# Optimization experiments

Hardware: AMD Instinct MI355X
Metric: run time of the kernel (lower is better)

Reference implementation:

```python
import jax, jax.numpy as jnp
import numpy as np

N = 100000   # nodes
C = 128      # channels
K = 16       # clusters
E = 3200000  # edges (avg degree 32)


def setup_inputs() -> dict:
    key = jax.random.key(0)
    k1, k2, k3, k4 = jax.random.split(key, 4)
    features = jax.random.normal(k1, (N, C), dtype=jnp.float32)
    edge_row = jax.random.randint(k2, (E,), 0, N, dtype=jnp.int32)
    edge_col = jax.random.randint(k3, (E,), 0, N, dtype=jnp.int32)
    edge_val = jnp.ones((E,), dtype=jnp.float32)
    # orthogonal-ish init for fc weight (matches nn.init.orthogonal_ in spirit)
    w = jax.random.normal(k4, (K, C), dtype=jnp.float32)
    q, _ = jnp.linalg.qr(w.T)          # [C, K], orthonormal columns
    fc_w = q.T.astype(jnp.float32)     # [K, C]
    fc_b = jnp.zeros((K,), dtype=jnp.float32)
    return {"features": features, "edge_row": edge_row, "edge_col": edge_col,
            "edge_val": edge_val, "fc_w": fc_w, "fc_b": fc_b}


def reference(features, edge_row, edge_col, edge_val, fc_w, fc_b):
    collapse_regularization = 1.0
    n_nodes = features.shape[0]
    n_clusters = fc_w.shape[0]

    # assignments = softmax(Linear(features))  -> [N, K]
    assignments = jax.nn.softmax(features @ fc_w.T + fc_b, axis=1)
    cluster_sizes = jnp.sum(assignments, axis=0)            # [K]
    assignments_pooling = assignments / cluster_sizes       # [N, K]

    # degrees = column sums of sparse adjacency (no densification)
    degrees = jax.ops.segment_sum(edge_val, edge_col, num_segments=n_nodes)  # [N]
    number_of_edges = jnp.sum(degrees)

    # sparse A @ assignments via segment_sum over edges -> [N, K]
    a_s = jax.ops.segment_sum(edge_val[:, None] * assignments[edge_col],
                              edge_row, num_segments=n_nodes)
    graph_pooled = a_s.T @ assignments                      # S^T A S, [K, K]

    normalizer_left = assignments.T @ degrees[:, None]      # [K, 1]
    normalizer_right = degrees[None, :] @ assignments       # [1, K]
    normalizer = (normalizer_left @ normalizer_right) / 2.0 / number_of_edges

    spectral_loss = -jnp.trace(graph_pooled - normalizer) / 2.0 / number_of_edges
    sk = np.sqrt(n_clusters).astype(np.float32)
    collapse_loss = (jnp.sum(jnp.abs(cluster_sizes - n_nodes / n_clusters))
                     / n_nodes * sk / (sk - 1.0) / 2.0)
    loss = spectral_loss + collapse_regularization * collapse_loss

    features_pooled = jax.nn.selu(assignments_pooling.T @ features)  # [K, C]
    features_pooled = assignments_pooling @ features_pooled          # unpool [N, C]
    return features_pooled, assignments, loss
```

## Files before the change

kernel.cpp:

```cpp
#include <hip/hip_runtime.h>
#include <hip/hip_fp16.h>
#include <math.h>


#define WS_ESUM 0
#define WS_TR   1
#define WS_M    2
#define WS_CS   18
#define WS_B    64
#define WS_P2   2112

#define OFF_AH  0
#define OFF_CSP 800000
#define OFF_EP  825008
#define OFF_BP  861872

typedef int   int4v   __attribute__((ext_vector_type(4)));
typedef float float4v __attribute__((ext_vector_type(4)));

__global__ __launch_bounds__(256) void k_assign(
    const float* __restrict__ F, const float* __restrict__ W,
    const float* __restrict__ bias, float* __restrict__ A,
    __half* __restrict__ Ah, float* __restrict__ csp, int N) {
  __shared__ float Ws[16 * 144];
  __shared__ float csred[4][16];
  int t = threadIdx.x;
#pragma unroll
  for (int i = 0; i < 8; i++) {
    int idx = t + 256 * i;
    int k = idx >> 7, r = idx & 127;
    Ws[k * 144 + (r >> 5) * 36 + (r & 31)] = W[idx];
  }
  __syncthreads();

  int p = t & 3;
  int slot = t >> 2;
  int n0 = blockIdx.x * 128 + slot;
  int n1 = n0 + 64;
  bool act0 = (n0 < N), act1 = (n1 < N);
  int n0c = act0 ? n0 : (N - 1);
  int n1c = act1 ? n1 : (N - 1);

  float a0[16], a1[16];
#pragma unroll
  for (int k = 0; k < 16; k++) { a0[k] = 0.f; a1[k] = 0.f; }

  const float4* f0 = (const float4*)(F + (size_t)n0c * 128 + p * 32);
  const float4* f1 = (const float4*)(F + (size_t)n1c * 128 + p * 32);
#pragma unroll
  for (int i = 0; i < 8; i++) {
    float4 x0 = f0[i];
    float4 x1 = f1[i];
#pragma unroll
    for (int k = 0; k < 16; k++) {
      float4 w = *(const float4*)(&Ws[k * 144 + p * 36 + i * 4]);
      a0[k] = fmaf(x0.x, w.x, a0[k]);
      a0[k] = fmaf(x0.y, w.y, a0[k]);
      a0[k] = fmaf(x0.z, w.z, a0[k]);
      a0[k] = fmaf(x0.w, w.w, a0[k]);
      a1[k] = fmaf(x1.x, w.x, a1[k]);
      a1[k] = fmaf(x1.y, w.y, a1[k]);
      a1[k] = fmaf(x1.z, w.z, a1[k]);
      a1[k] = fmaf(x1.w, w.w, a1[k]);
    }
  }

#pragma unroll
  for (int k = 0; k < 16; k++) {
    a0[k] += __shfl_xor(a0[k], 1, 64);
    a0[k] += __shfl_xor(a0[k], 2, 64);
    a1[k] += __shfl_xor(a1[k], 1, 64);
    a1[k] += __shfl_xor(a1[k], 2, 64);
  }

#pragma unroll
  for (int k = 0; k < 16; k++) { a0[k] += bias[k]; a1[k] += bias[k]; }

  float mx0 = a0[0], mx1 = a1[0];
#pragma unroll
  for (int k = 1; k < 16; k++) { mx0 = fmaxf(mx0, a0[k]); mx1 = fmaxf(mx1, a1[k]); }
  float s0 = 0.f, s1 = 0.f;
#pragma unroll
  for (int k = 0; k < 16; k++) {
    a0[k] = __expf(a0[k] - mx0); s0 += a0[k];
    a1[k] = __expf(a1[k] - mx1); s1 += a1[k];
  }
  float inv0 = 1.0f / s0, inv1 = 1.0f / s1;
#pragma unroll
  for (int k = 0; k < 16; k++) { a0[k] *= inv0; a1[k] *= inv1; }

  if (act0)
    ((float4*)(A + (size_t)n0 * 16))[p] =
        make_float4(a0[p * 4 + 0], a0[p * 4 + 1], a0[p * 4 + 2], a0[p * 4 + 3]);
  if (act1)
    ((float4*)(A + (size_t)n1 * 16))[p] =
        make_float4(a1[p * 4 + 0], a1[p * 4 + 1], a1[p * 4 + 2], a1[p * 4 + 3]);

  if (p == 0 && act0) {
    __half2 hh[4];
    hh[0].x = __float2half_rn(a0[0]); hh[0].y = __float2half_rn(a0[1]);
    hh[1].x = __float2half_rn(a0[2]); hh[1].y = __float2half_rn(a0[3]);
    hh[2].x = __float2half_rn(a0[4]); hh[2].y = __float2half_rn(a0[5]);
    hh[3].x = __float2half_rn(a0[6]); hh[3].y = __float2half_rn(a0[7]);
    *(uint4*)(Ah + (size_t)n0 * 16) = *(uint4*)hh;
  } else if (p == 1 && act0) {
    __half2 hh[4];
    hh[0].x = __float2half_rn(a0[8]);  hh[0].y = __float2half_rn(a0[9]);
    hh[1].x = __float2half_rn(a0[10]); hh[1].y = __float2half_rn(a0[11]);
    hh[2].x = __float2half_rn(a0[12]); hh[2].y = __float2half_rn(a0[13]);
    hh[3].x = __float2half_rn(a0[14]); hh[3].y = __float2half_rn(a0[15]);
    *(uint4*)(Ah + (size_t)n0 * 16 + 8) = *(uint4*)hh;
  } else if (p == 2 && act1) {
    __half2 hh[4];
    hh[0].x = __float2half_rn(a1[0]); hh[0].y = __float2half_rn(a1[1]);
    hh[1].x = __float2half_rn(a1[2]); hh[1].y = __float2half_rn(a1[3]);
    hh[2].x = __float2half_rn(a1[4]); hh[2].y = __float2half_rn(a1[5]);
    hh[3].x = __float2half_rn(a1[6]); hh[3].y = __float2half_rn(a1[7]);
    *(uint4*)(Ah + (size_t)n1 * 16) = *(uint4*)hh;
  } else if (p == 3 && act1) {
    __half2 hh[4];
    hh[0].x = __float2half_rn(a1[8]);  hh[0].y = __float2half_rn(a1[9]);
    hh[1].x = __float2half_rn(a1[10]); hh[1].y = __float2half_rn(a1[11]);
    hh[2].x = __float2half_rn(a1[12]); hh[2].y = __float2half_rn(a1[13]);
    hh[3].x = __float2half_rn(a1[14]); hh[3].y = __float2half_rn(a1[15]);
    *(uint4*)(Ah + (size_t)n1 * 16 + 8) = *(uint4*)hh;
  }

  int lane = t & 63, wid = t >> 6;
#pragma unroll
  for (int k = 0; k < 16; k++) {
    float v = 0.f;
    if (p == 0) {
      if (act0) v += a0[k];
      if (act1) v += a1[k];
    }
    for (int off = 32; off; off >>= 1) v += __shfl_xor(v, off, 64);
    if (lane == 0) csred[wid][k] = v;
  }
  __syncthreads();
  if (t < 16)
    csp[(size_t)blockIdx.x * 16 + t] =
        csred[0][t] + csred[1][t] + csred[2][t] + csred[3][t];
}

union H2F4 { float4 f4; __half2 h2[4]; };

__device__ __forceinline__ void edge_body(
    const __half* __restrict__ Ah, int r, int c, float v,
    float& eS, float& tr, float* m) {
  const float4* pc = (const float4*)(Ah + (size_t)c * 16);
  const float4* pr = (const float4*)(Ah + (size_t)r * 16);
  H2F4 uc0, uc1, ur0, ur1;
  uc0.f4 = pc[0]; uc1.f4 = pc[1];
  ur0.f4 = pr[0]; ur1.f4 = pr[1];
  float cf[16], rf[16];
#pragma unroll
  for (int j = 0; j < 4; j++) {
    float2 f;
    f = __half22float2(uc0.h2[j]); cf[2 * j] = f.x; cf[2 * j + 1] = f.y;
    f = __half22float2(uc1.h2[j]); cf[8 + 2 * j] = f.x; cf[9 + 2 * j] = f.y;
    f = __half22float2(ur0.h2[j]); rf[2 * j] = f.x; rf[2 * j + 1] = f.y;
    f = __half22float2(ur1.h2[j]); rf[8 + 2 * j] = f.x; rf[9 + 2 * j] = f.y;
  }
  eS += v;
  float d = 0.f;
#pragma unroll
  for (int k = 0; k < 16; k++) {
    m[k] = fmaf(v, cf[k], m[k]);
    d = fmaf(rf[k], cf[k], d);
  }
  tr = fmaf(v, d, tr);
}

__device__ __forceinline__ void group4(
    const __half* __restrict__ Ah, const int* __restrict__ row,
    const int* __restrict__ col, const float* __restrict__ val, int e,
    float& eS, float& tr, float* m) {
  int4v   ri = __builtin_nontemporal_load((const int4v*)(row + e));
  int4v   ci = __builtin_nontemporal_load((const int4v*)(col + e));
  float4v vi = __builtin_nontemporal_load((const float4v*)(val + e));

  H2F4 CA[4][2], RA[4][2];
#pragma unroll
  for (int j = 0; j < 4; j++) {
    const float4* pc = (const float4*)(Ah + (size_t)ci[j] * 16);
    const float4* pr = (const float4*)(Ah + (size_t)ri[j] * 16);
    CA[j][0].f4 = pc[0]; CA[j][1].f4 = pc[1];
    RA[j][0].f4 = pr[0]; RA[j][1].f4 = pr[1];
  }

#pragma unroll
  for (int j = 0; j < 4; j++) {
    float vj = vi[j];
    float cf[16], rf[16];
#pragma unroll
    for (int q = 0; q < 4; q++) {
      float2 f;
      f = __half22float2(CA[j][0].h2[q]); cf[2 * q] = f.x; cf[2 * q + 1] = f.y;
      f = __half22float2(CA[j][1].h2[q]); cf[8 + 2 * q] = f.x; cf[9 + 2 * q] = f.y;
      f = __half22float2(RA[j][0].h2[q]); rf[2 * q] = f.x; rf[2 * q + 1] = f.y;
      f = __half22float2(RA[j][1].h2[q]); rf[8 + 2 * q] = f.x; rf[9 + 2 * q] = f.y;
    }
    eS += vj;
    float d = 0.f;
#pragma unroll
    for (int k = 0; k < 16; k++) {
      m[k] = fmaf(vj, cf[k], m[k]);
      d = fmaf(rf[k], cf[k], d);
    }
    tr = fmaf(vj, d, tr);
  }
}

__global__ __launch_bounds__(256) void k_edge(
    const int* __restrict__ row, const int* __restrict__ col,
    const float* __restrict__ val, const __half* __restrict__ Ah,
    float* __restrict__ ep, int E) {
  float eS = 0.f, tr = 0.f;
  float m[16];
#pragma unroll
  for (int i = 0; i < 16; i++) m[i] = 0.f;

  int gid = blockIdx.x * 256 + threadIdx.x;
  int T4 = gridDim.x * 256 * 4;
  int E4 = E & ~3;
  for (int e = gid * 4; e < E4; e += T4)
    group4(Ah, row, col, val, e, eS, tr, m);
  if (gid < E - E4)
    edge_body(Ah, row[E4 + gid], col[E4 + gid], val[E4 + gid], eS, tr, m);

  float vals[18];
  vals[0] = eS; vals[1] = tr;
#pragma unroll
  for (int i = 0; i < 16; i++) vals[2 + i] = m[i];
#pragma unroll
  for (int i = 0; i < 18; i++) {
    float v = vals[i];
    for (int off = 32; off; off >>= 1) v += __shfl_xor(v, off, 64);
    vals[i] = v;
  }
  __shared__ float red[4][18];
  int lane = threadIdx.x & 63, wid = threadIdx.x >> 6;
  if (lane == 0) {
#pragma unroll
    for (int i = 0; i < 18; i++) red[wid][i] = vals[i];
  }
  __syncthreads();
  if (threadIdx.x < 18)
    ep[(size_t)blockIdx.x * 18 + threadIdx.x] =
        red[0][threadIdx.x] + red[1][threadIdx.x] +
        red[2][threadIdx.x] + red[3][threadIdx.x];
}

__global__ __launch_bounds__(256) void k_nodeB(
    const float* __restrict__ F, const float* __restrict__ A,
    float* __restrict__ bp, int N) {
  int t = threadIdx.x;
  int q = t & 31;
  int sub = t >> 5;

  float4 acc[16];
#pragma unroll
  for (int k = 0; k < 16; k++) acc[k] = make_float4(0.f, 0.f, 0.f, 0.f);

  const float4* F4 = (const float4*)F;
  const float4* A4 = (const float4*)A;
  int stride = gridDim.x * 8;
  for (int n = blockIdx.x * 8 + sub; n < N; n += stride) {
    float4 f  = F4[(size_t)n * 32 + q];
    float4 a0 = A4[(size_t)n * 4 + 0];
    float4 a1 = A4[(size_t)n * 4 + 1];
    float4 a2 = A4[(size_t)n * 4 + 2];
    float4 a3 = A4[(size_t)n * 4 + 3];
    float av[16] = {a0.x, a0.y, a0.z, a0.w, a1.x, a1.y, a1.z, a1.w,
                    a2.x, a2.y, a2.z, a2.w, a3.x, a3.y, a3.z, a3.w};
#pragma unroll
    for (int k = 0; k < 16; k++) {
      acc[k].x = fmaf(av[k], f.x, acc[k].x);
      acc[k].y = fmaf(av[k], f.y, acc[k].y);
      acc[k].z = fmaf(av[k], f.z, acc[k].z);
      acc[k].w = fmaf(av[k], f.w, acc[k].w);
    }
  }

#pragma unroll
  for (int k = 0; k < 16; k++) {
    acc[k].x += __shfl_xor(acc[k].x, 32, 64);
    acc[k].y += __shfl_xor(acc[k].y, 32, 64);
    acc[k].z += __shfl_xor(acc[k].z, 32, 64);
    acc[k].w += __shfl_xor(acc[k].w, 32, 64);
  }

  __shared__ float red[4][2048];
  int lane = t & 63, wid = t >> 6;
  if (lane < 32) {
#pragma unroll
    for (int k = 0; k < 16; k++)
      *(float4*)&red[wid][k * 128 + q * 4] = acc[k];
  }
  __syncthreads();
  float* myp = bp + (size_t)blockIdx.x * 2048;
#pragma unroll
  for (int qq = 0; qq < 2; qq++) {
    int base = t * 8 + qq * 4;
    float4 s0 = *(float4*)&red[0][base];
    float4 s1 = *(float4*)&red[1][base];
    float4 s2 = *(float4*)&red[2][base];
    float4 s3 = *(float4*)&red[3][base];
    *(float4*)&myp[base] = make_float4(s0.x + s1.x + s2.x + s3.x,
                                       s0.y + s1.y + s2.y + s3.y,
                                       s0.z + s1.z + s2.z + s3.z,
                                       s0.w + s1.w + s2.w + s3.w);
  }
}

__global__ __launch_bounds__(256) void k_reduce(
    const float* __restrict__ csp, const float* __restrict__ ep,
    const float* __restrict__ bp, float* __restrict__ ws,
    int GA, int GE, int GB) {
  __shared__ float L[256];
  int t = threadIdx.x;
  int b = blockIdx.x;
  if (b < 256) {
    int cell = b * 8 + (t & 7);
    int seg = t >> 3;
    float s0 = 0.f, s1 = 0.f, s2 = 0.f, s3 = 0.f;
    int g = seg;
    for (; g + 96 < GB; g += 128) {
      s0 += bp[(size_t)g * 2048 + cell];
      s1 += bp[(size_t)(g + 32) * 2048 + cell];
      s2 += bp[(size_t)(g + 64) * 2048 + cell];
      s3 += bp[(size_t)(g + 96) * 2048 + cell];
    }
    for (; g < GB; g += 32) s0 += bp[(size_t)g * 2048 + cell];
    L[t] = (s0 + s1) + (s2 + s3);
    __syncthreads();
    if (t < 8) {
      float tot = 0.f;
#pragma unroll
      for (int s = 0; s < 32; s++) tot += L[s * 8 + t];
      ws[WS_B + b * 8 + t] = tot;
    }
  } else if (b == 256) {
    int n = GE * 18;
    float s0 = 0.f, s1 = 0.f, s2 = 0.f, s3 = 0.f;
    if (t < 252) {
      int f = t;
      for (; f + 756 < n; f += 1008) {
        s0 += ep[f]; s1 += ep[f + 252]; s2 += ep[f + 504]; s3 += ep[f + 756];
      }
      for (; f < n; f += 252) s0 += ep[f];
    }
    L[t] = (s0 + s1) + (s2 + s3);
    __syncthreads();
    if (t < 18) {
      float tot = 0.f;
#pragma unroll
      for (int j = 0; j < 14; j++) tot += L[j * 18 + t];
      ws[t] = tot;
    }
  } else {
    int n = GA * 16;
    float s0 = 0.f, s1 = 0.f, s2 = 0.f, s3 = 0.f;
    int f = t;
    for (; f + 768 < n; f += 1024) {
      s0 += csp[f]; s1 += csp[f + 256]; s2 += csp[f + 512]; s3 += csp[f + 768];
    }
    for (; f < n; f += 256) s0 += csp[f];
    L[t] = (s0 + s1) + (s2 + s3);
    __syncthreads();
    if (t < 16) {
      float tot = 0.f;
#pragma unroll
      for (int j = 0; j < 16; j++) tot += L[j * 16 + t];
      ws[WS_CS + t] = tot;
    }
  }
}

__global__ __launch_bounds__(256) void k_finalize(
    float* __restrict__ ws, float* __restrict__ loss_out, int N) {
  __shared__ float invcs[16];
  int t = threadIdx.x;
  if (t < 16) invcs[t] = 1.0f / ws[WS_CS + t];
  __syncthreads();
  const float* B = ws + WS_B;
  float* P2 = ws + WS_P2;
  const float scale = 1.0507009873554805f;
  const float alpha = 1.6732632423543772f;
#pragma unroll
  for (int idx = t; idx < 2048; idx += 256) {
    int k = idx >> 7;
    float x = B[idx] * invcs[k];
    float s = (x > 0.f) ? scale * x : scale * alpha * expm1f(x);
    P2[idx] = s * invcs[k];
  }
  if (t == 0) {
    float Es = ws[WS_ESUM], tr = ws[WS_TR];
    float m2 = 0.f;
#pragma unroll
    for (int i = 0; i < 16; i++) m2 += ws[WS_M + i] * ws[WS_M + i];
    float spectral = -(tr - m2 / (2.0f * Es)) / (2.0f * Es);
    float coll = 0.f;
    float tgt = (float)N / 16.0f;
#pragma unroll
    for (int i = 0; i < 16; i++) coll += fabsf(ws[WS_CS + i] - tgt);
    coll = coll / (float)N * (4.0f / 3.0f / 2.0f);
    loss_out[0] = spectral + coll;
  }
}

__global__ __launch_bounds__(256) void k_unpool(
    const float* __restrict__ A, const float* __restrict__ P2,
    float* __restrict__ out, int N) {
  __shared__ float Ps[2048];
  int t = threadIdx.x;
#pragma unroll
  for (int i = 0; i < 8; i++) Ps[t + 256 * i] = P2[t + 256 * i];
  __syncthreads();
  int c4 = (t & 31) << 2;
  int sub = t >> 5;
  float4 pk[16];
#pragma unroll
  for (int k = 0; k < 16; k++) pk[k] = *(const float4*)&Ps[k * 128 + c4];

  int stride = gridDim.x * 8;
  for (int n = blockIdx.x * 8 + sub; n < N; n += stride) {
    const float4* a4 = (const float4*)(A + (size_t)n * 16);
    float4 a0 = a4[0], a1 = a4[1], a2 = a4[2], a3 = a4[3];
    float av[16] = {a0.x, a0.y, a0.z, a0.w, a1.x, a1.y, a1.z, a1.w,
                    a2.x, a2.y, a2.z, a2.w, a3.x, a3.y, a3.z, a3.w};
    float4 s = make_float4(0.f, 0.f, 0.f, 0.f);
#pragma unroll
    for (int k = 0; k < 16; k++) {
      s.x = fmaf(av[k], pk[k].x, s.x);
      s.y = fmaf(av[k], pk[k].y, s.y);
      s.z = fmaf(av[k], pk[k].z, s.z);
      s.w = fmaf(av[k], pk[k].w, s.w);
    }
    *(float4*)(out + (size_t)n * 128 + c4) = s;
  }
}

extern "C" void kernel_launch(void* const* d_in, const int* in_sizes, int n_in,
                              void* d_out, int out_size, void* d_ws, size_t ws_size,
                              hipStream_t stream) {
  const float* F    = (const float*)d_in[0];
  const int*   erow = (const int*)d_in[1];
  const int*   ecol = (const int*)d_in[2];
  const float* eval_= (const float*)d_in[3];
  const float* W    = (const float*)d_in[4];
  const float* bias = (const float*)d_in[5];

  int N = in_sizes[0] / 128;
  int E = in_sizes[1];

  float* out0 = (float*)d_out;
  float* A    = out0 + (size_t)N * 128;
  float* loss = A + (size_t)N * 16;
  float* ws   = (float*)d_ws;

  int GA = (N + 127) / 128;
  int GE = 1563;
  int GB = 1024;

  __half* Ah  = (__half*)(out0 + OFF_AH);
  float*  csp = out0 + OFF_CSP;
  float*  ep  = out0 + OFF_EP;
  float*  bp  = out0 + OFF_BP;

  k_assign<<<GA, 256, 0, stream>>>(F, W, bias, A, Ah, csp, N);
  k_edge<<<GE, 256, 0, stream>>>(erow, ecol, eval_, Ah, ep, E);
  k_nodeB<<<GB, 256, 0, stream>>>(F, A, bp, N);
  k_reduce<<<258, 256, 0, stream>>>(csp, ep, bp, ws, GA, GE, GB);
  k_finalize<<<1, 256, 0, stream>>>(ws, loss, N);
  k_unpool<<<1280, 256, 0, stream>>>(A, ws + WS_P2, out0, N);
}
```

Before: 260.2 us.

## Fuse edge and node-pooling kernels into one launch and fold finalize into unpool

Merges the edge-gather kernel and the features-pooling kernel into a single launch, interleaving node blocks (every fifth block) with edge blocks so the two memory-bound phases run concurrently. Each node-block wave now writes its own partial row with no LDS reduction, which quadruples the partial rows k_reduce has to sum. The edge loop now does scalar per-thread edges with 2x unroll instead of vector groups of 4. The finalize kernel is folded into unpool: every block recomputes the SELU-pooled matrix, and the unpool output uses nontemporal stores. Together these remove two launches at the cost of redundant per-block work and more partial-sum traffic.

```diff
diff --git a/kernel.cpp b/kernel.cpp
--- a/kernel.cpp
+++ b/kernel.cpp
@@ -8,14 +8,17 @@
 #define WS_M    2
 #define WS_CS   18
 #define WS_B    64
-#define WS_P2   2112
 
 #define OFF_AH  0
 #define OFF_CSP 800000
 #define OFF_EP  825008
 #define OFF_BP  861872
 
+#define GE_BLOCKS 2048
+#define GB_BLOCKS 512
+
 typedef int   int4v   __attribute__((ext_vector_type(4)));
+typedef float float2v __attribute__((ext_vector_type(2)));
 typedef float float4v __attribute__((ext_vector_type(4)));
 
 __global__ __launch_bounds__(256) void k_assign(
@@ -172,145 +175,88 @@
   tr = fmaf(v, d, tr);
 }
 
-__device__ __forceinline__ void group4(
-    const __half* __restrict__ Ah, const int* __restrict__ row,
-    const int* __restrict__ col, const float* __restrict__ val, int e,
-    float& eS, float& tr, float* m) {
-  int4v   ri = __builtin_nontemporal_load((const int4v*)(row + e));
-  int4v   ci = __builtin_nontemporal_load((const int4v*)(col + e));
-  float4v vi = __builtin_nontemporal_load((const float4v*)(val + e));
-
-  H2F4 CA[4][2], RA[4][2];
-#pragma unroll
-  for (int j = 0; j < 4; j++) {
-    const float4* pc = (const float4*)(Ah + (size_t)ci[j] * 16);
-    const float4* pr = (const float4*)(Ah + (size_t)ri[j] * 16);
-    CA[j][0].f4 = pc[0]; CA[j][1].f4 = pc[1];
-    RA[j][0].f4 = pr[0]; RA[j][1].f4 = pr[1];
-  }
-
-#pragma unroll
-  for (int j = 0; j < 4; j++) {
-    float vj = vi[j];
-    float cf[16], rf[16];
-#pragma unroll
-    for (int q = 0; q < 4; q++) {
-      float2 f;
-      f = __half22float2(CA[j][0].h2[q]); cf[2 * q] = f.x; cf[2 * q + 1] = f.y;
-      f = __half22float2(CA[j][1].h2[q]); cf[8 + 2 * q] = f.x; cf[9 + 2 * q] = f.y;
-      f = __half22float2(RA[j][0].h2[q]); rf[2 * q] = f.x; rf[2 * q + 1] = f.y;
-      f = __half22float2(RA[j][1].h2[q]); rf[8 + 2 * q] = f.x; rf[9 + 2 * q] = f.y;
-    }
-    eS += vj;
-    float d = 0.f;
-#pragma unroll
-    for (int k = 0; k < 16; k++) {
-      m[k] = fmaf(vj, cf[k], m[k]);
-      d = fmaf(rf[k], cf[k], d);
-    }
-    tr = fmaf(vj, d, tr);
-  }
-}
-
-__global__ __launch_bounds__(256) void k_edge(
+__global__ __launch_bounds__(256, 8) void k_edge_nodeB(
     const int* __restrict__ row, const int* __restrict__ col,
     const float* __restrict__ val, const __half* __restrict__ Ah,
-    float* __restrict__ ep, int E) {
-  float eS = 0.f, tr = 0.f;
-  float m[16];
-#pragma unroll
-  for (int i = 0; i < 16; i++) m[i] = 0.f;
-
-  int gid = blockIdx.x * 256 + threadIdx.x;
-  int T4 = gridDim.x * 256 * 4;
-  int E4 = E & ~3;
-  for (int e = gid * 4; e < E4; e += T4)
-    group4(Ah, row, col, val, e, eS, tr, m);
-  if (gid < E - E4)
-    edge_body(Ah, row[E4 + gid], col[E4 + gid], val[E4 + gid], eS, tr, m);
-
-  float vals[18];
-  vals[0] = eS; vals[1] = tr;
-#pragma unroll
-  for (int i = 0; i < 16; i++) vals[2 + i] = m[i];
-#pragma unroll
-  for (int i = 0; i < 18; i++) {
-    float v = vals[i];
-    for (int off = 32; off; off >>= 1) v += __shfl_xor(v, off, 64);
-    vals[i] = v;
-  }
+    const float* __restrict__ F, const float* __restrict__ A,
+    float* __restrict__ ep, float* __restrict__ bp, int E, int N) {
   __shared__ float red[4][18];
-  int lane = threadIdx.x & 63, wid = threadIdx.x >> 6;
-  if (lane == 0) {
-#pragma unroll
-    for (int i = 0; i < 18; i++) red[wid][i] = vals[i];
-  }
-  __syncthreads();
-  if (threadIdx.x < 18)
-    ep[(size_t)blockIdx.x * 18 + threadIdx.x] =
-        red[0][threadIdx.x] + red[1][threadIdx.x] +
-        red[2][threadIdx.x] + red[3][threadIdx.x];
-}
-
-__global__ __launch_bounds__(256) void k_nodeB(
-    const float* __restrict__ F, const float* __restrict__ A,
-    float* __restrict__ bp, int N) {
+  int b = blockIdx.x;
   int t = threadIdx.x;
-  int q = t & 31;
-  int sub = t >> 5;
-
-  float4 acc[16];
-#pragma unroll
-  for (int k = 0; k < 16; k++) acc[k] = make_float4(0.f, 0.f, 0.f, 0.f);
-
-  const float4* F4 = (const float4*)F;
-  const float4* A4 = (const float4*)A;
-  int stride = gridDim.x * 8;
-  for (int n = blockIdx.x * 8 + sub; n < N; n += stride) {
-    float4 f  = F4[(size_t)n * 32 + q];
-    float4 a0 = A4[(size_t)n * 4 + 0];
-    float4 a1 = A4[(size_t)n * 4 + 1];
-    float4 a2 = A4[(size_t)n * 4 + 2];
-    float4 a3 = A4[(size_t)n * 4 + 3];
-    float av[16] = {a0.x, a0.y, a0.z, a0.w, a1.x, a1.y, a1.z, a1.w,
-                    a2.x, a2.y, a2.z, a2.w, a3.x, a3.y, a3.z, a3.w};
-#pragma unroll
-    for (int k = 0; k < 16; k++) {
-      acc[k].x = fmaf(av[k], f.x, acc[k].x);
-      acc[k].y = fmaf(av[k], f.y, acc[k].y);
-      acc[k].z = fmaf(av[k], f.z, acc[k].z);
-      acc[k].w = fmaf(av[k], f.w, acc[k].w);
-    }
-  }
-
-#pragma unroll
-  for (int k = 0; k < 16; k++) {
-    acc[k].x += __shfl_xor(acc[k].x, 32, 64);
-    acc[k].y += __shfl_xor(acc[k].y, 32, 64);
-    acc[k].z += __shfl_xor(acc[k].z, 32, 64);
-    acc[k].w += __shfl_xor(acc[k].w, 32, 64);
-  }
-
-  __shared__ float red[4][2048];
-  int lane = t & 63, wid = t >> 6;
-  if (lane < 32) {
+  bool isNode = ((b % 5) == 4);
+
+  if (!isNode) {
+    int eb = b - b / 5;
+    float eS = 0.f, tr = 0.f;
+    float m[16];
+#pragma unroll
+    for (int i = 0; i < 16; i++) m[i] = 0.f;
+
+    int tid = eb * 256 + t;
+    const int T = GE_BLOCKS * 256;
+    int e = tid;
+    for (; e + T < E; e += 2 * T) {
+      int   r0 = __builtin_nontemporal_load(row + e);
+      int   c0 = __builtin_nontemporal_load(col + e);
+      int   r1 = __builtin_nontemporal_load(row + e + T);
+      int   c1 = __builtin_nontemporal_load(col + e + T);
+      float v0 = __builtin_nontemporal_load(val + e);
+      float v1 = __builtin_nontemporal_load(val + e + T);
+      edge_body(Ah, r0, c0, v0, eS, tr, m);
+      edge_body(Ah, r1, c1, v1, eS, tr, m);
+    }
+    for (; e < E; e += T)
+      edge_body(Ah, row[e], col[e], val[e], eS, tr, m);
+
+    float vals[18];
+    vals[0] = eS; vals[1] = tr;
+#pragma unroll
+    for (int i = 0; i < 16; i++) vals[2 + i] = m[i];
+#pragma unroll
+    for (int i = 0; i < 18; i++) {
+      float v = vals[i];
+      for (int off = 32; off; off >>= 1) v += __shfl_xor(v, off, 64);
+      vals[i] = v;
+    }
+    int lane = t & 63, wid = t >> 6;
+    if (lane == 0) {
+#pragma unroll
+      for (int i = 0; i < 18; i++) red[wid][i] = vals[i];
+    }
+    __syncthreads();
+    if (t < 18)
+      ep[(size_t)eb * 18 + t] =
+          red[0][t] + red[1][t] + red[2][t] + red[3][t];
+  } else {
+    int nb = b / 5;
+    int lane = t & 63;
+    int wid = t >> 6;
+
+    float2 acc[16];
+#pragma unroll
+    for (int k = 0; k < 16; k++) acc[k] = make_float2(0.f, 0.f);
+
+    const float2v* F2 = (const float2v*)F;
+    const float4* A4 = (const float4*)A;
+    const int stride = GB_BLOCKS * 4;
+    for (int n = nb * 4 + wid; n < N; n += stride) {
+      float2v f = __builtin_nontemporal_load(&F2[(size_t)n * 64 + lane]);
+      float4 a0 = A4[(size_t)n * 4 + 0];
+      float4 a1 = A4[(size_t)n * 4 + 1];
+      float4 a2 = A4[(size_t)n * 4 + 2];
+      float4 a3 = A4[(size_t)n * 4 + 3];
+      float av[16] = {a0.x, a0.y, a0.z, a0.w, a1.x, a1.y, a1.z, a1.w,
+                      a2.x, a2.y, a2.z, a2.w, a3.x, a3.y, a3.z, a3.w};
+#pragma unroll
+      for (int k = 0; k < 16; k++) {
+        acc[k].x = fmaf(av[k], f.x, acc[k].x);
+        acc[k].y = fmaf(av[k], f.y, acc[k].y);
+      }
+    }
+    float* myrow = bp + (size_t)(nb * 4 + wid) * 2048;
 #pragma unroll
     for (int k = 0; k < 16; k++)
-      *(float4*)&red[wid][k * 128 + q * 4] = acc[k];
-  }
-  __syncthreads();
-  float* myp = bp + (size_t)blockIdx.x * 2048;
-#pragma unroll
-  for (int qq = 0; qq < 2; qq++) {
-    int base = t * 8 + qq * 4;
-    float4 s0 = *(float4*)&red[0][base];
-    float4 s1 = *(float4*)&red[1][base];
-    float4 s2 = *(float4*)&red[2][base];
-    float4 s3 = *(float4*)&red[3][base];
-    *(float4*)&myp[base] = make_float4(s0.x + s1.x + s2.x + s3.x,
-                                       s0.y + s1.y + s2.y + s3.y,
-                                       s0.z + s1.z + s2.z + s3.z,
-                                       s0.w + s1.w + s2.w + s3.w);
+      *(float2*)&myrow[k * 128 + lane * 2] = acc[k];
   }
 }
 
@@ -378,24 +324,27 @@
   }
 }
 
-__global__ __launch_bounds__(256) void k_finalize(
-    float* __restrict__ ws, float* __restrict__ loss_out, int N) {
+__global__ __launch_bounds__(256) void k_unpool(
+    const float* __restrict__ A, float* __restrict__ ws,
+    float* __restrict__ out, float* __restrict__ loss_out, int N) {
+  __shared__ float Ps[2048];
   __shared__ float invcs[16];
   int t = threadIdx.x;
   if (t < 16) invcs[t] = 1.0f / ws[WS_CS + t];
   __syncthreads();
-  const float* B = ws + WS_B;
-  float* P2 = ws + WS_P2;
   const float scale = 1.0507009873554805f;
   const float alpha = 1.6732632423543772f;
 #pragma unroll
-  for (int idx = t; idx < 2048; idx += 256) {
+  for (int i = 0; i < 8; i++) {
+    int idx = t + 256 * i;
     int k = idx >> 7;
-    float x = B[idx] * invcs[k];
+    float x = ws[WS_B + idx] * invcs[k];
     float s = (x > 0.f) ? scale * x : scale * alpha * expm1f(x);
-    P2[idx] = s * invcs[k];
-  }
-  if (t == 0) {
+    Ps[idx] = s * invcs[k];
+  }
+  __syncthreads();
+
+  if (blockIdx.x == 0 && t == 0) {
     float Es = ws[WS_ESUM], tr = ws[WS_TR];
     float m2 = 0.f;
 #pragma unroll
@@ -408,16 +357,7 @@
     coll = coll / (float)N * (4.0f / 3.0f / 2.0f);
     loss_out[0] = spectral + coll;
   }
-}
-
-__global__ __launch_bounds__(256) void k_unpool(
-    const float* __restrict__ A, const float* __restrict__ P2,
-    float* __restrict__ out, int N) {
-  __shared__ float Ps[2048];
-  int t = threadIdx.x;
-#pragma unroll
-  for (int i = 0; i < 8; i++) Ps[t + 256 * i] = P2[t + 256 * i];
-  __syncthreads();
+
   int c4 = (t & 31) << 2;
   int sub = t >> 5;
   float4 pk[16];
@@ -430,7 +370,7 @@
     float4 a0 = a4[0], a1 = a4[1], a2 = a4[2], a3 = a4[3];
     float av[16] = {a0.x, a0.y, a0.z, a0.w, a1.x, a1.y, a1.z, a1.w,
                     a2.x, a2.y, a2.z, a2.w, a3.x, a3.y, a3.z, a3.w};
-    float4 s = make_float4(0.f, 0.f, 0.f, 0.f);
+    float4v s = {0.f, 0.f, 0.f, 0.f};
 #pragma unroll
     for (int k = 0; k < 16; k++) {
       s.x = fmaf(av[k], pk[k].x, s.x);
@@ -438,7 +378,7 @@
       s.z = fmaf(av[k], pk[k].z, s.z);
       s.w = fmaf(av[k], pk[k].w, s.w);
     }
-    *(float4*)(out + (size_t)n * 128 + c4) = s;
+    __builtin_nontemporal_store(s, (float4v*)(out + (size_t)n * 128 + c4));
   }
 }
 
@@ -461,8 +401,8 @@
   float* ws   = (float*)d_ws;
 
   int GA = (N + 127) / 128;
-  int GE = 1563;
-  int GB = 1024;
+  int GE = GE_BLOCKS;
+  int GBp = GB_BLOCKS * 4;
 
   __half* Ah  = (__half*)(out0 + OFF_AH);
   float*  csp = out0 + OFF_CSP;
@@ -470,9 +410,8 @@
   float*  bp  = out0 + OFF_BP;
 
   k_assign<<<GA, 256, 0, stream>>>(F, W, bias, A, Ah, csp, N);
-  k_edge<<<GE, 256, 0, stream>>>(erow, ecol, eval_, Ah, ep, E);
-  k_nodeB<<<GB, 256, 0, stream>>>(F, A, bp, N);
-  k_reduce<<<258, 256, 0, stream>>>(csp, ep, bp, ws, GA, GE, GB);
-  k_finalize<<<1, 256, 0, stream>>>(ws, loss, N);
-  k_unpool<<<1280, 256, 0, stream>>>(A, ws + WS_P2, out0, N);
-}
+  k_edge_nodeB<<<GE_BLOCKS + GB_BLOCKS, 256, 0, stream>>>(
+      erow, ecol, eval_, Ah, F, A, ep, bp, E, N);
+  k_reduce<<<258, 256, 0, stream>>>(csp, ep, bp, ws, GA, GE, GBp);
+  k_unpool<<<1280, 256, 0, stream>>>(A, ws, out0, loss, N);
+}
```

Result: faster. 246.8 us (-5.1%).
